# Optimization experiments

Measured on AMD Instinct MI355X. Metric: run time of the kernel, lower is better.

The kernel has to match this reference:

```python
import jax, jax.numpy as jnp
import numpy as np

N = 10000   # nodes
E = 40000   # edges
D = 256     # d_model
H = 32      # num_heads
DK = 16     # d_k == d_v
L = 5       # decoder layers
SQRT_DK = float(np.sqrt(DK))


def layer_norm(x, g, b, eps=1e-5):
    m = x.mean(-1, keepdims=True)
    v = ((x - m) ** 2).mean(-1, keepdims=True)
    return (x - m) / jnp.sqrt(v + eps) * g + b


def mha(x, edge_index, We, Wq, Wk, Wv, Wo, bo):
    # x: [N, D]
    xe = x @ We.T                                   # embed, no bias
    Q = (xe @ Wq.T).reshape(N, H, DK)               # [N, H, dk]
    K = (xe @ Wk.T).reshape(N, H, DK)
    V = (xe @ Wv.T).reshape(N, H, DK)
    src, dst = edge_index[0], edge_index[1]          # message j->i, aggregate at dst
    Qi = Q[dst]                                      # [E, H, dk]
    Kj = K[src]
    Vj = V[src]
    # torch split_heads gives [*, dk, H]; Q_i @ K_j^T contracts over the HEAD axis
    alpha = jnp.einsum('eha,ehb->eab', Qi, Kj) / SQRT_DK   # [E, dk, dk]
    att = jax.nn.softmax(alpha, axis=-1)                    # per-edge softmax over last dk axis
    msg = jnp.einsum('eab,ehb->eah', att, Vj)               # [E, dk, H]
    agg = jax.ops.segment_sum(msg, dst, num_segments=N)     # [N, dk, H] scatter-add
    attn_out = jnp.transpose(agg, (0, 2, 1)).reshape(N, H * DK)  # combine_heads
    # dropout is identity at inference
    return xe + attn_out @ Wo.T + bo


def decoder(edge_index, x, We, Wq, Wk, Wv, Wo, bo, ln_g, ln_b, mlp_W, mlp_b):
    for l in range(L):
        h = mha(x, edge_index, We[l, 0], Wq[l, 0], Wk[l, 0], Wv[l, 0], Wo[l, 0], bo[l, 0])
        x = layer_norm(x + h, ln_g[l, 0], ln_b[l, 0])
        h = mha(x, edge_index, We[l, 1], Wq[l, 1], Wk[l, 1], Wv[l, 1], Wo[l, 1], bo[l, 1])
        x = layer_norm(x + h, ln_g[l, 1], ln_b[l, 1])
        x = layer_norm(x + x @ mlp_W[l].T + mlp_b[l], ln_g[l, 2], ln_b[l, 2])
    return x


def setup_inputs() -> dict:
    key = jax.random.key(0)
    ks = jax.random.split(key, 10)
    s = 0.05
    return {
        'edge_index': jax.random.randint(ks[0], (2, E), 0, N, dtype=jnp.int32),
        'x': jax.random.normal(ks[1], (N, D), dtype=jnp.float32),
        'We': jax.random.normal(ks[2], (L, 2, D, D), dtype=jnp.float32) * s,
        'Wq': jax.random.normal(ks[3], (L, 2, H * DK, D), dtype=jnp.float32) * s,
        'Wk': jax.random.normal(ks[4], (L, 2, H * DK, D), dtype=jnp.float32) * s,
        'Wv': jax.random.normal(ks[5], (L, 2, H * DK, D), dtype=jnp.float32) * s,
        'Wo': jax.random.normal(ks[6], (L, 2, D, H * DK), dtype=jnp.float32) * s,
        'bo': jnp.zeros((L, 2, D), dtype=jnp.float32),
        'ln_g': jnp.ones((L, 3, D), dtype=jnp.float32),
        'ln_b': jnp.zeros((L, 3, D), dtype=jnp.float32),
        'mlp_W': jax.random.normal(ks[7], (L, D, D), dtype=jnp.float32) * s,
        'mlp_b': jnp.zeros((L, D), dtype=jnp.float32),
    }


def reference(edge_index, x, We, Wq, Wk, Wv, Wo, bo, ln_g, ln_b, mlp_W, mlp_b):
    return decoder(edge_index, x, We, Wq, Wk, Wv, Wo, bo, ln_g, ln_b, mlp_W, mlp_b)
```

## Files before the change

### kernel.cpp

```cpp
#include <hip/hip_runtime.h>
#include <hip/hip_bf16.h>

#define N_NODES 10000
#define N_EDGES 40000
#define NLAYERS 5

typedef __bf16 bf16x8 __attribute__((ext_vector_type(8)));
typedef __bf16 bf16x4 __attribute__((ext_vector_type(4)));
typedef float  f32x4  __attribute__((ext_vector_type(4)));

__device__ __forceinline__ bf16x8 cvt8(float4 a, float4 b) {
    bf16x8 r;
    r[0] = (__bf16)a.x; r[1] = (__bf16)a.y; r[2] = (__bf16)a.z; r[3] = (__bf16)a.w;
    r[4] = (__bf16)b.x; r[5] = (__bf16)b.y; r[6] = (__bf16)b.z; r[7] = (__bf16)b.w;
    return r;
}

__device__ __forceinline__ void gload_lds16(const void* g, void* l) {
    __builtin_amdgcn_global_load_lds(
        (const __attribute__((address_space(1))) void*)g,
        (__attribute__((address_space(3))) void*)l, 16, 0, 0);
}

__global__ __launch_bounds__(256) void cvt_chunks(
    const float* __restrict__ s, __bf16* __restrict__ d,
    long chunk, long dstStride, long total8)
{
    for (long i = (long)blockIdx.x * blockDim.x + threadIdx.x; i < total8;
         i += (long)gridDim.x * blockDim.x) {
        long e = i * 8;
        long ch = e / chunk;
        long r  = e - ch * chunk;
        float4 a = *(const float4*)(s + e);
        float4 b = *(const float4*)(s + e + 4);
        *(bf16x8*)(d + ch * dstStride + r) = cvt8(a, b);
    }
}

__global__ __launch_bounds__(256) void cvt_perm_qk(
    const float* __restrict__ S, __bf16* __restrict__ D, long total8)
{
    for (long i = (long)blockIdx.x * blockDim.x + threadIdx.x; i < total8;
         i += (long)gridDim.x * blockDim.x) {
        long e = i * 8;
        int slot = (int)(e >> 17);
        int rem  = (int)(e & 131071);
        int row  = rem >> 8;
        int col  = rem & 255;
        int srow = ((row & 31) << 4) | (row >> 5);
        const float* sp = S + ((long)slot << 17) + ((long)srow << 8) + col;
        float4 a = *(const float4*)sp;
        float4 b = *(const float4*)(sp + 4);
        *(bf16x8*)(D + (long)slot * 393216 + ((long)row << 8) + col) = cvt8(a, b);
    }
}

__global__ __launch_bounds__(256) void transpose_we(
    const float* __restrict__ S, __bf16* __restrict__ D)
{
    __shared__ float tile[64][65];
    const int slot = blockIdx.y;
    const int tx = blockIdx.x & 3, ty = blockIdx.x >> 2;
    const float* sp = S + (size_t)slot * 65536 + (size_t)(ty * 64) * 256 + tx * 64;
    const int t = threadIdx.x;
    #pragma unroll
    for (int j = 0; j < 16; ++j) {
        int idx = t + 256 * j;
        int r = idx >> 6, c = idx & 63;
        tile[r][c] = sp[r * 256 + c];
    }
    __syncthreads();
    __bf16* dp = D + (size_t)slot * 65536 + (size_t)(tx * 64) * 256 + ty * 64;
    #pragma unroll
    for (int j = 0; j < 16; ++j) {
        int idx = t + 256 * j;
        int nl = idx >> 6, kl = idx & 63;
        dp[nl * 256 + kl] = (__bf16)tile[kl][nl];
    }
}

__global__ __launch_bounds__(256) void hist_dst(
    const int* __restrict__ eidx, int* __restrict__ counts)
{
    int e = blockIdx.x * 256 + threadIdx.x;
    if (e < N_EDGES) atomicAdd(&counts[eidx[N_EDGES + e]], 1);
}

__global__ __launch_bounds__(256) void scan_offsets(
    const int* __restrict__ counts, int* __restrict__ offs,
    int* __restrict__ wrk, int n)
{
    const int tid = threadIdx.x;
    const int base = tid * 40;
    int local[40];
    int s = 0;
    #pragma unroll
    for (int j = 0; j < 40; ++j) {
        int i = base + j;
        int v = (i < n) ? counts[i] : 0;
        local[j] = s; s += v;
    }
    __shared__ int sm[256];
    sm[tid] = s;
    __syncthreads();
    for (int off = 1; off < 256; off <<= 1) {
        int t2 = (tid >= off) ? sm[tid - off] : 0;
        __syncthreads();
        sm[tid] += t2;
        __syncthreads();
    }
    int pre = (tid == 0) ? 0 : sm[tid - 1];
    #pragma unroll
    for (int j = 0; j < 40; ++j) {
        int i = base + j;
        if (i < n) { int v = pre + local[j]; offs[i] = v; wrk[i] = v; }
    }
    if (tid == 255) offs[n] = sm[255];
}

__global__ __launch_bounds__(256) void scatter_csr(
    const int* __restrict__ eidx, int* __restrict__ wrk, int* __restrict__ csr_src)
{
    int e = blockIdx.x * 256 + threadIdx.x;
    if (e < N_EDGES) {
        int sn = eidx[e];
        int d  = eidx[N_EDGES + e];
        int pos = atomicAdd(&wrk[d], 1);
        csr_src[pos] = sn;
    }
}

template<int MODE, int BN>
__global__ __launch_bounds__(256) void gemm_lds(
    const __bf16* __restrict__ A, const __bf16* __restrict__ W,
    float* __restrict__ Cf, __bf16* __restrict__ Ch,
    int M, int K, int ldc, long sA, long sW, long sC)
{
    __shared__ __bf16 As[128 * 64];
    __shared__ __bf16 Wsh[BN * 64];
    constexpr int NF = BN / 32;
    A += (long)blockIdx.z * sA;
    W += (long)blockIdx.z * sW;
    if (Ch) Ch += (long)blockIdx.z * sC;
    const int tid = threadIdx.x;
    const int ln  = tid & 63;
    const int wv  = tid >> 6;
    const int wr  = wv >> 1, wc = wv & 1;
    const int brow0 = blockIdx.y * 128;
    const int colb0 = blockIdx.x * BN;

    const int srow = ln >> 3;
    const int scol = ((ln & 7) ^ srow) * 8;
    const int fr = ln & 15;
    const int kq = ln >> 4;
    char* asb = (char*)As;
    char* wsb = (char*)Wsh;

    f32x4 acc[4][NF];
    #pragma unroll
    for (int m = 0; m < 4; ++m)
        #pragma unroll
        for (int n = 0; n < NF; ++n) acc[m][n] = (f32x4){0.f, 0.f, 0.f, 0.f};

    const int nt = K >> 6;
    for (int t = 0; t < nt; ++t) {
        const int kk0 = t << 6;
        if (t) __syncthreads();
        #pragma unroll
        for (int c = 0; c < 4; ++c) {
            int ch = wv * 4 + c;
            int grow = brow0 + ch * 8 + srow;
            if (grow >= M) grow = M - 1;
            gload_lds16(A + (size_t)grow * K + kk0 + scol, asb + ch * 1024);
        }
        #pragma unroll
        for (int c = 0; c < NF; ++c) {
            int ch = wv * NF + c;
            int grow = colb0 + ch * 8 + srow;
            gload_lds16(W + (size_t)grow * K + kk0 + scol, wsb + ch * 1024);
        }
        __syncthreads();
        #pragma unroll
        for (int ks = 0; ks < 2; ++ks) {
            const int kb = ks * 64 + kq * 16;
            const int sw = (fr & 7) << 4;
            bf16x8 af[4], wf[NF];
            #pragma unroll
            for (int m = 0; m < 4; ++m) {
                int row = wr * 64 + m * 16 + fr;
                af[m] = *(const bf16x8*)(asb + row * 128 + (kb ^ sw));
            }
            #pragma unroll
            for (int n = 0; n < NF; ++n) {
                int row = wc * (BN / 2) + n * 16 + fr;
                wf[n] = *(const bf16x8*)(wsb + row * 128 + (kb ^ sw));
            }
            #pragma unroll
            for (int m = 0; m < 4; ++m)
                #pragma unroll
                for (int n = 0; n < NF; ++n)
                    acc[m][n] = __builtin_amdgcn_mfma_f32_16x16x32_bf16(
                        af[m], wf[n], acc[m][n], 0, 0, 0);
        }
    }

    const int rq = (ln >> 4) * 4;
    #pragma unroll
    for (int m = 0; m < 4; ++m) {
        #pragma unroll
        for (int rr = 0; rr < 4; ++rr) {
            int orow = brow0 + wr * 64 + m * 16 + rq + rr;
            if (orow < M) {
                #pragma unroll
                for (int n = 0; n < NF; ++n) {
                    int c = colb0 + wc * (BN / 2) + fr + n * 16;
                    if (MODE == 0)      Cf[(size_t)orow * ldc + c] = acc[m][n][rr];
                    else if (MODE == 1) Ch[(size_t)orow * ldc + c] = (__bf16)acc[m][n][rr];
                    else {
                        if (c < 256) Ch[(size_t)orow * 256 + c] = (__bf16)acc[m][n][rr];
                        else ((__bf16*)Cf)[(size_t)orow * 1536 + (c - 256)] = (__bf16)acc[m][n][rr];
                    }
                }
            }
        }
    }
}

__global__ __launch_bounds__(256) void edge_attn_csr(
    const int* __restrict__ csr_off, const int* __restrict__ csr_src,
    const __bf16* __restrict__ qkv, __bf16* __restrict__ attn_bf)
{
    const int lane = threadIdx.x & 63;
    const int d = blockIdx.x * 4 + (threadIdx.x >> 6);
    const int fr = lane & 15;
    const int G  = lane >> 4;

    const __bf16* qT = qkv + (size_t)d * 1536;
    const bf16x8 qf = *(const bf16x8*)(qT + fr * 32 + G * 8);

    const f32x4 zero = {0.f, 0.f, 0.f, 0.f};
    f32x4 acc0 = zero, acc1 = zero;

    const int i0 = csr_off[d], i1 = csr_off[d + 1];
    for (int i = i0; i < i1; ++i) {
        const int s = csr_src[i];
        const __bf16* kT = qkv + (size_t)s * 1536 + 512;
        const __bf16* vp = qkv + (size_t)s * 1536 + 1024;

        bf16x8 kf = *(const bf16x8*)(kT + fr * 32 + G * 8);
        f32x4 al = __builtin_amdgcn_mfma_f32_16x16x32_bf16(kf, qf, zero, 0, 0, 0);

        float mx = fmaxf(fmaxf(al[0], al[1]), fmaxf(al[2], al[3]));
        mx = fmaxf(mx, __shfl_xor(mx, 16));
        mx = fmaxf(mx, __shfl_xor(mx, 32));
        float p[4];
        #pragma unroll
        for (int r = 0; r < 4; ++r) p[r] = __expf((al[r] - mx) * 0.25f);
        float sum = p[0] + p[1] + p[2] + p[3];
        sum += __shfl_xor(sum, 16);
        sum += __shfl_xor(sum, 32);
        const float inv = 1.f / sum;

        bf16x8 paf;
        #pragma unroll
        for (int j = 0; j < 8; ++j) {
            int srcLane = fr + ((G * 8 + j) >> 2) * 16;
            float v = __shfl(p[j & 3], srcLane);
            paf[j] = (G < 2) ? (__bf16)(v * inv) : (__bf16)0.f;
        }

        bf16x8 vf0 = {0, 0, 0, 0, 0, 0, 0, 0};
        bf16x8 vf1 = {0, 0, 0, 0, 0, 0, 0, 0};
        if (G < 2) {
            vf0 = *(const bf16x8*)(vp + fr * 16 + G * 8);
            vf1 = *(const bf16x8*)(vp + (16 + fr) * 16 + G * 8);
        }
        acc0 = __builtin_amdgcn_mfma_f32_16x16x32_bf16(paf, vf0, acc0, 0, 0, 0);
        acc1 = __builtin_amdgcn_mfma_f32_16x16x32_bf16(paf, vf1, acc1, 0, 0, 0);
    }

    __bf16* ob = attn_bf + (size_t)d * 512;
    bf16x4 o0, o1;
    #pragma unroll
    for (int r = 0; r < 4; ++r) { o0[r] = (__bf16)acc0[r]; o1[r] = (__bf16)acc1[r]; }
    *(bf16x4*)(ob + fr * 16 + G * 4)       = o0;
    *(bf16x4*)(ob + 256 + fr * 16 + G * 4) = o1;
}

template<bool HAS_TB>
__global__ __launch_bounds__(256) void fused_gemm_ln(
    const __bf16* __restrict__ A, const __bf16* __restrict__ W,
    const float* __restrict__ xres, const __bf16* __restrict__ tb,
    const float* __restrict__ bias, const float* __restrict__ g,
    const float* __restrict__ b, float* __restrict__ outf,
    __bf16* __restrict__ outb, int M, int K)
{
    __shared__ __bf16 As[32 * 64];
    __shared__ __bf16 Wsh[256 * 64];
    __shared__ float sm_s[4][32];
    __shared__ float sm_q[4][32];
    const int tid = threadIdx.x;
    const int ln  = tid & 63;
    const int wv  = tid >> 6;
    const int brow0 = blockIdx.x * 32;
    const int srow = ln >> 3;
    const int scol = ((ln & 7) ^ srow) * 8;
    const int fr = ln & 15;
    const int kq = ln >> 4;
    char* asb = (char*)As;
    char* wsb = (char*)Wsh;

    f32x4 acc[2][4];
    #pragma unroll
    for (int m = 0; m < 2; ++m)
        #pragma unroll
        for (int n = 0; n < 4; ++n) acc[m][n] = (f32x4){0.f, 0.f, 0.f, 0.f};

    const int nt = K >> 6;
    for (int t = 0; t < nt; ++t) {
        const int kk0 = t << 6;
        if (t) __syncthreads();
        {
            int grow = brow0 + wv * 8 + srow;
            if (grow >= M) grow = M - 1;
            gload_lds16(A + (size_t)grow * K + kk0 + scol, asb + wv * 1024);
        }
        #pragma unroll
        for (int c = 0; c < 8; ++c) {
            int ch = wv * 8 + c;
            int grow = ch * 8 + srow;
            gload_lds16(W + (size_t)grow * K + kk0 + scol, wsb + ch * 1024);
        }
        __syncthreads();
        #pragma unroll
        for (int ks = 0; ks < 2; ++ks) {
            const int kb = ks * 64 + kq * 16;
            const int sw = (fr & 7) << 4;
            bf16x8 af0 = *(const bf16x8*)(asb + fr * 128 + (kb ^ sw));
            bf16x8 af1 = *(const bf16x8*)(asb + (16 + fr) * 128 + (kb ^ sw));
            #pragma unroll
            for (int n = 0; n < 4; ++n) {
                bf16x8 wf = *(const bf16x8*)(wsb + (wv * 64 + n * 16 + fr) * 128 + (kb ^ sw));
                acc[0][n] = __builtin_amdgcn_mfma_f32_16x16x32_bf16(af0, wf, acc[0][n], 0, 0, 0);
                acc[1][n] = __builtin_amdgcn_mfma_f32_16x16x32_bf16(af1, wf, acc[1][n], 0, 0, 0);
            }
        }
    }

    float s[2][4], q[2][4];
    #pragma unroll
    for (int m = 0; m < 2; ++m)
        #pragma unroll
        for (int rr = 0; rr < 4; ++rr) { s[m][rr] = 0.f; q[m][rr] = 0.f; }
    #pragma unroll
    for (int m = 0; m < 2; ++m)
        #pragma unroll
        for (int n = 0; n < 4; ++n) {
            const int col = wv * 64 + n * 16 + fr;
            const float bi = bias[col];
            #pragma unroll
            for (int rr = 0; rr < 4; ++rr) {
                int gr = brow0 + m * 16 + kq * 4 + rr; if (gr >= M) gr = M - 1;
                float v = acc[m][n][rr] + xres[(size_t)gr * 256 + col] + bi;
                if (HAS_TB) v += (float)tb[(size_t)gr * 256 + col];
                acc[m][n][rr] = v;
                s[m][rr] += v; q[m][rr] += v * v;
            }
        }
    #pragma unroll
    for (int mask = 1; mask < 16; mask <<= 1)
        #pragma unroll
        for (int m = 0; m < 2; ++m)
            #pragma unroll
            for (int rr = 0; rr < 4; ++rr) {
                s[m][rr] += __shfl_xor(s[m][rr], mask);
                q[m][rr] += __shfl_xor(q[m][rr], mask);
            }
    if (fr == 0) {
        #pragma unroll
        for (int m = 0; m < 2; ++m)
            #pragma unroll
            for (int rr = 0; rr < 4; ++rr) {
                sm_s[wv][m * 16 + kq * 4 + rr] = s[m][rr];
                sm_q[wv][m * 16 + kq * 4 + rr] = q[m][rr];
            }
    }
    __syncthreads();
    float mean[2][4], invs[2][4];
    #pragma unroll
    for (int m = 0; m < 2; ++m)
        #pragma unroll
        for (int rr = 0; rr < 4; ++rr) {
            int r = m * 16 + kq * 4 + rr;
            float ts = sm_s[0][r] + sm_s[1][r] + sm_s[2][r] + sm_s[3][r];
            float tq = sm_q[0][r] + sm_q[1][r] + sm_q[2][r] + sm_q[3][r];
            float mn = ts * (1.f / 256.f);
            mean[m][rr] = mn;
            invs[m][rr] = rsqrtf(tq * (1.f / 256.f) - mn * mn + 1e-5f);
        }
    #pragma unroll
    for (int m = 0; m < 2; ++m)
        #pragma unroll
        for (int n = 0; n < 4; ++n) {
            const int col = wv * 64 + n * 16 + fr;
            const float gv = g[col], bv = b[col];
            #pragma unroll
            for (int rr = 0; rr < 4; ++rr) {
                int gr = brow0 + m * 16 + kq * 4 + rr;
                if (gr < M) {
                    float o = (acc[m][n][rr] - mean[m][rr]) * invs[m][rr] * gv + bv;
                    outf[(size_t)gr * 256 + col] = o;
                    outb[(size_t)gr * 256 + col] = (__bf16)o;
                }
            }
        }
}

extern "C" void kernel_launch(void* const* d_in, const int* in_sizes, int n_in,
                              void* d_out, int out_size, void* d_ws, size_t ws_size,
                              hipStream_t stream)
{
    const int*   eidx = (const int*)  d_in[0];
    const float* x_in = (const float*)d_in[1];
    const float* We   = (const float*)d_in[2];
    const float* Wq   = (const float*)d_in[3];
    const float* Wk   = (const float*)d_in[4];
    const float* Wv   = (const float*)d_in[5];
    const float* Wo   = (const float*)d_in[6];
    const float* bo   = (const float*)d_in[7];
    const float* lng  = (const float*)d_in[8];
    const float* lnb  = (const float*)d_in[9];
    const float* mlpW = (const float*)d_in[10];
    const float* mlpb = (const float*)d_in[11];
    float* out = (float*)d_out;

    char* p = (char*)d_ws;
    __bf16* wMerged = (__bf16*)p; p += (size_t)10 * 458752 * 2;
    __bf16* wQKVtmp = (__bf16*)p; p += (size_t)10 * 393216 * 2;
    __bf16* wET     = (__bf16*)p; p += (size_t)10 * 65536  * 2;
    __bf16* wO      = (__bf16*)p; p += (size_t)10 * 131072 * 2;
    __bf16* wM      = (__bf16*)p; p += (size_t)5  * 65536  * 2;
    __bf16* qkv     = (__bf16*)p; p += (size_t)N_NODES * 1536 * 2;
    __bf16* attn_bf = (__bf16*)p; p += (size_t)N_NODES * 512 * 2;
    __bf16* xeb     = (__bf16*)p; p += (size_t)N_NODES * 256 * 2;
    float*  xbf     = (float*) p; p += (size_t)N_NODES * 256 * 4;
    __bf16* xbb     = (__bf16*)p; p += (size_t)N_NODES * 256 * 2;
    int* counts  = (int*)p;    p += (size_t)(N_NODES + 16) * 4;
    int* csr_off = (int*)p;    p += (size_t)(N_NODES + 16) * 4;
    int* csr_wrk = (int*)p;    p += (size_t)(N_NODES + 16) * 4;
    int* csr_src = (int*)p;    p += (size_t)N_EDGES * 4;
    if ((size_t)(p - (char*)d_ws) > ws_size) return;

    dim3 blk(256);
    auto cvtg = [](long total8) { long g = (total8 + 255) / 256; return dim3((unsigned)(g > 2048 ? 2048 : g)); };

    hipMemsetAsync(counts, 0, (size_t)(N_NODES + 16) * 4, stream);
    hist_dst<<<dim3(157), blk, 0, stream>>>(eidx, counts);
    scan_offsets<<<dim3(1), blk, 0, stream>>>(counts, csr_off, csr_wrk, N_NODES);
    scatter_csr<<<dim3(157), blk, 0, stream>>>(eidx, csr_wrk, csr_src);

    cvt_chunks<<<cvtg(81920), blk, 0, stream>>>(We, wMerged, 65536, 458752, 81920);
    cvt_perm_qk<<<cvtg(163840), blk, 0, stream>>>(Wq, wQKVtmp,          163840);
    cvt_perm_qk<<<cvtg(163840), blk, 0, stream>>>(Wk, wQKVtmp + 131072, 163840);
    cvt_chunks<<<cvtg(163840), blk, 0, stream>>>(Wv, wQKVtmp + 262144, 131072, 393216, 163840);
    transpose_we<<<dim3(16, 10), blk, 0, stream>>>(We, wET);
    cvt_chunks<<<cvtg(163840), blk, 0, stream>>>(Wo,  wO, 131072, 131072, 163840);
    cvt_chunks<<<cvtg(40960), blk, 0, stream>>>(mlpW, wM, 65536, 65536, 40960);
    cvt_chunks<<<cvtg(320000), blk, 0, stream>>>(x_in, xbb, 2560000, 2560000, 320000);

    gemm_lds<1, 64><<<dim3(4, 12, 10), blk, 0, stream>>>(
        wQKVtmp, wET, nullptr, wMerged + 65536, 1536, 256, 256,
        393216, 65536, 458752);

    dim3 gMerged(14, 79);

    const float* xcur_f = x_in;
    int step = 0;
    for (int l = 0; l < NLAYERS; ++l) {
        for (int s = 0; s < 2; ++s) {
            size_t ls = (size_t)(l * 2 + s);
            gemm_lds<3, 128><<<gMerged, blk, 0, stream>>>(
                xbb, wMerged + ls * 458752, (float*)qkv, xeb, N_NODES, 256, 0, 0, 0, 0);
            edge_attn_csr<<<dim3(N_NODES / 4), blk, 0, stream>>>(csr_off, csr_src,
                                                                 qkv, attn_bf);
            bool last = (step == 14);
            fused_gemm_ln<true><<<dim3(313), blk, 0, stream>>>(
                attn_bf, wO + ls * 131072, xcur_f, xeb, bo + ls * 256,
                lng + (size_t)(l * 3 + s) * 256, lnb + (size_t)(l * 3 + s) * 256,
                last ? out : xbf, xbb, N_NODES, 512);
            xcur_f = xbf; ++step;
        }
        bool last = (step == 14);
        fused_gemm_ln<false><<<dim3(313), blk, 0, stream>>>(
            xbb, wM + (size_t)l * 65536, xcur_f, nullptr, mlpb + (size_t)l * 256,
            lng + (size_t)(l * 3 + 2) * 256, lnb + (size_t)(l * 3 + 2) * 256,
            last ? out : xbf, xbb, N_NODES, 256);
        xcur_f = xbf; ++step;
    }
}
```

Before: 759.0 us.

## Fuse edge attention into output projection+LayerNorm kernel and merge weight conversions

The per-edge attention kernel is merged into the Wo GEMM + LayerNorm kernel, so each 512-thread block computes attention for 32 destination nodes into LDS and immediately projects and normalizes them. This removes the attn_bf global round trip and one launch per MHA. The MLP GEMM+LN becomes a separate 512-thread kernel that loads A once into LDS and reads W directly from global. The seven weight and input conversion launches are merged into one 2D-grid kernel. In exchange, the fused kernel has only 313 blocks and serializes four nodes' edge loops per wave, which may reduce latency hiding in the gather phase. It also reads W from global without LDS staging.

```diff
diff --git a/kernel.cpp b/kernel.cpp
--- a/kernel.cpp
+++ b/kernel.cpp
@@ -22,36 +22,59 @@
         (__attribute__((address_space(3))) void*)l, 16, 0, 0);
 }
 
-__global__ __launch_bounds__(256) void cvt_chunks(
-    const float* __restrict__ s, __bf16* __restrict__ d,
-    long chunk, long dstStride, long total8)
-{
-    for (long i = (long)blockIdx.x * blockDim.x + threadIdx.x; i < total8;
-         i += (long)gridDim.x * blockDim.x) {
-        long e = i * 8;
-        long ch = e / chunk;
-        long r  = e - ch * chunk;
-        float4 a = *(const float4*)(s + e);
-        float4 b = *(const float4*)(s + e + 4);
-        *(bf16x8*)(d + ch * dstStride + r) = cvt8(a, b);
-    }
-}
-
-__global__ __launch_bounds__(256) void cvt_perm_qk(
-    const float* __restrict__ S, __bf16* __restrict__ D, long total8)
-{
-    for (long i = (long)blockIdx.x * blockDim.x + threadIdx.x; i < total8;
-         i += (long)gridDim.x * blockDim.x) {
-        long e = i * 8;
-        int slot = (int)(e >> 17);
-        int rem  = (int)(e & 131071);
-        int row  = rem >> 8;
-        int col  = rem & 255;
-        int srow = ((row & 31) << 4) | (row >> 5);
-        const float* sp = S + ((long)slot << 17) + ((long)srow << 8) + col;
-        float4 a = *(const float4*)sp;
-        float4 b = *(const float4*)(sp + 4);
-        *(bf16x8*)(D + (long)slot * 393216 + ((long)row << 8) + col) = cvt8(a, b);
+__global__ __launch_bounds__(256) void prep_cvt(
+    const float* __restrict__ We, const float* __restrict__ Wq,
+    const float* __restrict__ Wk, const float* __restrict__ Wv,
+    const float* __restrict__ Wo, const float* __restrict__ mlpW,
+    const float* __restrict__ x_in,
+    __bf16* __restrict__ wMerged, __bf16* __restrict__ wQKVtmp,
+    __bf16* __restrict__ wOd, __bf16* __restrict__ wMd, __bf16* __restrict__ xbb)
+{
+    const int reg = blockIdx.y;
+    long i0 = (long)blockIdx.x * blockDim.x + threadIdx.x;
+    long stride = (long)gridDim.x * blockDim.x;
+    if (reg == 0) {
+        for (long i = i0; i < 81920; i += stride) {
+            long e = i * 8; long ch = e >> 16; long r = e & 65535;
+            *(bf16x8*)(wMerged + ch * 458752 + r) =
+                cvt8(*(const float4*)(We + e), *(const float4*)(We + e + 4));
+        }
+    } else if (reg == 1 || reg == 2) {
+        const float* S = (reg == 1) ? Wq : Wk;
+        __bf16* D = wQKVtmp + ((reg == 2) ? 131072 : 0);
+        for (long i = i0; i < 163840; i += stride) {
+            long e = i * 8;
+            int slot = (int)(e >> 17); int rem = (int)(e & 131071);
+            int row = rem >> 8; int col = rem & 255;
+            int srow = ((row & 31) << 4) | (row >> 5);
+            const float* sp = S + ((long)slot << 17) + ((long)srow << 8) + col;
+            *(bf16x8*)(D + (long)slot * 393216 + ((long)row << 8) + col) =
+                cvt8(*(const float4*)sp, *(const float4*)(sp + 4));
+        }
+    } else if (reg == 3) {
+        for (long i = i0; i < 163840; i += stride) {
+            long e = i * 8; long ch = e >> 17; long r = e & 131071;
+            *(bf16x8*)(wQKVtmp + 262144 + ch * 393216 + r) =
+                cvt8(*(const float4*)(Wv + e), *(const float4*)(Wv + e + 4));
+        }
+    } else if (reg == 4) {
+        for (long i = i0; i < 163840; i += stride) {
+            long e = i * 8;
+            *(bf16x8*)(wOd + e) =
+                cvt8(*(const float4*)(Wo + e), *(const float4*)(Wo + e + 4));
+        }
+    } else if (reg == 5) {
+        for (long i = i0; i < 40960; i += stride) {
+            long e = i * 8;
+            *(bf16x8*)(wMd + e) =
+                cvt8(*(const float4*)(mlpW + e), *(const float4*)(mlpW + e + 4));
+        }
+    } else {
+        for (long i = i0; i < 320000; i += stride) {
+            long e = i * 8;
+            *(bf16x8*)(xbb + e) =
+                cvt8(*(const float4*)(x_in + e), *(const float4*)(x_in + e + 4));
+        }
     }
 }
 
@@ -226,145 +249,123 @@
     }
 }
 
-__global__ __launch_bounds__(256) void edge_attn_csr(
+__global__ __launch_bounds__(512) void mha_tail(
     const int* __restrict__ csr_off, const int* __restrict__ csr_src,
-    const __bf16* __restrict__ qkv, __bf16* __restrict__ attn_bf)
-{
-    const int lane = threadIdx.x & 63;
-    const int d = blockIdx.x * 4 + (threadIdx.x >> 6);
-    const int fr = lane & 15;
-    const int G  = lane >> 4;
-
-    const __bf16* qT = qkv + (size_t)d * 1536;
-    const bf16x8 qf = *(const bf16x8*)(qT + fr * 32 + G * 8);
-
-    const f32x4 zero = {0.f, 0.f, 0.f, 0.f};
-    f32x4 acc0 = zero, acc1 = zero;
-
-    const int i0 = csr_off[d], i1 = csr_off[d + 1];
-    for (int i = i0; i < i1; ++i) {
-        const int s = csr_src[i];
-        const __bf16* kT = qkv + (size_t)s * 1536 + 512;
-        const __bf16* vp = qkv + (size_t)s * 1536 + 1024;
-
-        bf16x8 kf = *(const bf16x8*)(kT + fr * 32 + G * 8);
-        f32x4 al = __builtin_amdgcn_mfma_f32_16x16x32_bf16(kf, qf, zero, 0, 0, 0);
-
-        float mx = fmaxf(fmaxf(al[0], al[1]), fmaxf(al[2], al[3]));
-        mx = fmaxf(mx, __shfl_xor(mx, 16));
-        mx = fmaxf(mx, __shfl_xor(mx, 32));
-        float p[4];
-        #pragma unroll
-        for (int r = 0; r < 4; ++r) p[r] = __expf((al[r] - mx) * 0.25f);
-        float sum = p[0] + p[1] + p[2] + p[3];
-        sum += __shfl_xor(sum, 16);
-        sum += __shfl_xor(sum, 32);
-        const float inv = 1.f / sum;
-
-        bf16x8 paf;
-        #pragma unroll
-        for (int j = 0; j < 8; ++j) {
-            int srcLane = fr + ((G * 8 + j) >> 2) * 16;
-            float v = __shfl(p[j & 3], srcLane);
-            paf[j] = (G < 2) ? (__bf16)(v * inv) : (__bf16)0.f;
-        }
-
-        bf16x8 vf0 = {0, 0, 0, 0, 0, 0, 0, 0};
-        bf16x8 vf1 = {0, 0, 0, 0, 0, 0, 0, 0};
-        if (G < 2) {
-            vf0 = *(const bf16x8*)(vp + fr * 16 + G * 8);
-            vf1 = *(const bf16x8*)(vp + (16 + fr) * 16 + G * 8);
-        }
-        acc0 = __builtin_amdgcn_mfma_f32_16x16x32_bf16(paf, vf0, acc0, 0, 0, 0);
-        acc1 = __builtin_amdgcn_mfma_f32_16x16x32_bf16(paf, vf1, acc1, 0, 0, 0);
-    }
-
-    __bf16* ob = attn_bf + (size_t)d * 512;
-    bf16x4 o0, o1;
-    #pragma unroll
-    for (int r = 0; r < 4; ++r) { o0[r] = (__bf16)acc0[r]; o1[r] = (__bf16)acc1[r]; }
-    *(bf16x4*)(ob + fr * 16 + G * 4)       = o0;
-    *(bf16x4*)(ob + 256 + fr * 16 + G * 4) = o1;
-}
-
-template<bool HAS_TB>
-__global__ __launch_bounds__(256) void fused_gemm_ln(
-    const __bf16* __restrict__ A, const __bf16* __restrict__ W,
+    const __bf16* __restrict__ qkv, const __bf16* __restrict__ W,
     const float* __restrict__ xres, const __bf16* __restrict__ tb,
     const float* __restrict__ bias, const float* __restrict__ g,
     const float* __restrict__ b, float* __restrict__ outf,
-    __bf16* __restrict__ outb, int M, int K)
-{
-    __shared__ __bf16 As[32 * 64];
-    __shared__ __bf16 Wsh[256 * 64];
-    __shared__ float sm_s[4][32];
-    __shared__ float sm_q[4][32];
+    __bf16* __restrict__ outb, int M)
+{
+    __shared__ __bf16 attn_s[32 * 512];
+    __shared__ float sm_s[8][32];
+    __shared__ float sm_q[8][32];
     const int tid = threadIdx.x;
     const int ln  = tid & 63;
     const int wv  = tid >> 6;
+    const int fr  = ln & 15;
+    const int kq  = ln >> 4;
     const int brow0 = blockIdx.x * 32;
-    const int srow = ln >> 3;
-    const int scol = ((ln & 7) ^ srow) * 8;
-    const int fr = ln & 15;
-    const int kq = ln >> 4;
-    char* asb = (char*)As;
-    char* wsb = (char*)Wsh;
-
-    f32x4 acc[2][4];
-    #pragma unroll
-    for (int m = 0; m < 2; ++m)
-        #pragma unroll
-        for (int n = 0; n < 4; ++n) acc[m][n] = (f32x4){0.f, 0.f, 0.f, 0.f};
-
-    const int nt = K >> 6;
-    for (int t = 0; t < nt; ++t) {
-        const int kk0 = t << 6;
-        if (t) __syncthreads();
-        {
-            int grow = brow0 + wv * 8 + srow;
-            if (grow >= M) grow = M - 1;
-            gload_lds16(A + (size_t)grow * K + kk0 + scol, asb + wv * 1024);
-        }
-        #pragma unroll
-        for (int c = 0; c < 8; ++c) {
-            int ch = wv * 8 + c;
-            int grow = ch * 8 + srow;
-            gload_lds16(W + (size_t)grow * K + kk0 + scol, wsb + ch * 1024);
-        }
-        __syncthreads();
+    char* asb = (char*)attn_s;
+    const f32x4 zero = {0.f, 0.f, 0.f, 0.f};
+
+    for (int j = 0; j < 4; ++j) {
+        const int r = wv * 4 + j;
+        const int d = brow0 + r;
+        if (d < M) {
+            const __bf16* qT = qkv + (size_t)d * 1536;
+            const bf16x8 qf = *(const bf16x8*)(qT + fr * 32 + kq * 8);
+            f32x4 acc0 = zero, acc1 = zero;
+            const int i0 = csr_off[d], i1 = csr_off[d + 1];
+            int sN = (i0 < i1) ? csr_src[i0] : 0;
+            bf16x8 kfN = *(const bf16x8*)(qkv + (size_t)sN * 1536 + 512 + fr * 32 + kq * 8);
+            for (int i = i0; i < i1; ++i) {
+                const int s = sN;
+                const bf16x8 kf = kfN;
+                if (i + 1 < i1) {
+                    sN = csr_src[i + 1];
+                    kfN = *(const bf16x8*)(qkv + (size_t)sN * 1536 + 512 + fr * 32 + kq * 8);
+                }
+                const __bf16* vp = qkv + (size_t)s * 1536 + 1024;
+                bf16x8 vf0 = {0, 0, 0, 0, 0, 0, 0, 0};
+                bf16x8 vf1 = {0, 0, 0, 0, 0, 0, 0, 0};
+                if (kq < 2) {
+                    vf0 = *(const bf16x8*)(vp + fr * 16 + kq * 8);
+                    vf1 = *(const bf16x8*)(vp + (16 + fr) * 16 + kq * 8);
+                }
+                f32x4 al = __builtin_amdgcn_mfma_f32_16x16x32_bf16(kf, qf, zero, 0, 0, 0);
+                float mx = fmaxf(fmaxf(al[0], al[1]), fmaxf(al[2], al[3]));
+                mx = fmaxf(mx, __shfl_xor(mx, 16));
+                mx = fmaxf(mx, __shfl_xor(mx, 32));
+                float p[4];
+                #pragma unroll
+                for (int rr = 0; rr < 4; ++rr) p[rr] = __expf((al[rr] - mx) * 0.25f);
+                float sum = p[0] + p[1] + p[2] + p[3];
+                sum += __shfl_xor(sum, 16);
+                sum += __shfl_xor(sum, 32);
+                const float inv = 1.f / sum;
+                bf16x8 paf;
+                #pragma unroll
+                for (int jj = 0; jj < 8; ++jj) {
+                    int srcLane = fr + ((kq * 8 + jj) >> 2) * 16;
+                    float v = __shfl(p[jj & 3], srcLane);
+                    paf[jj] = (kq < 2) ? (__bf16)(v * inv) : (__bf16)0.f;
+                }
+                acc0 = __builtin_amdgcn_mfma_f32_16x16x32_bf16(paf, vf0, acc0, 0, 0, 0);
+                acc1 = __builtin_amdgcn_mfma_f32_16x16x32_bf16(paf, vf1, acc1, 0, 0, 0);
+            }
+            bf16x4 o0, o1;
+            #pragma unroll
+            for (int rr = 0; rr < 4; ++rr) { o0[rr] = (__bf16)acc0[rr]; o1[rr] = (__bf16)acc1[rr]; }
+            const int sw = (r & 7) << 4;
+            *(bf16x4*)(asb + r * 1024 + ((fr * 32 + kq * 8) ^ sw))       = o0;
+            *(bf16x4*)(asb + r * 1024 + ((512 + fr * 32 + kq * 8) ^ sw)) = o1;
+        }
+    }
+    __syncthreads();
+
+    f32x4 acc[2][2];
+    #pragma unroll
+    for (int m = 0; m < 2; ++m)
+        #pragma unroll
+        for (int n = 0; n < 2; ++n) acc[m][n] = zero;
+    const int colw = wv * 32;
+    const int swr = (fr & 7) << 4;
+    #pragma unroll
+    for (int t = 0; t < 8; ++t) {
         #pragma unroll
         for (int ks = 0; ks < 2; ++ks) {
-            const int kb = ks * 64 + kq * 16;
-            const int sw = (fr & 7) << 4;
-            bf16x8 af0 = *(const bf16x8*)(asb + fr * 128 + (kb ^ sw));
-            bf16x8 af1 = *(const bf16x8*)(asb + (16 + fr) * 128 + (kb ^ sw));
-            #pragma unroll
-            for (int n = 0; n < 4; ++n) {
-                bf16x8 wf = *(const bf16x8*)(wsb + (wv * 64 + n * 16 + fr) * 128 + (kb ^ sw));
-                acc[0][n] = __builtin_amdgcn_mfma_f32_16x16x32_bf16(af0, wf, acc[0][n], 0, 0, 0);
-                acc[1][n] = __builtin_amdgcn_mfma_f32_16x16x32_bf16(af1, wf, acc[1][n], 0, 0, 0);
-            }
-        }
-    }
-
-    float s[2][4], q[2][4];
-    #pragma unroll
-    for (int m = 0; m < 2; ++m)
-        #pragma unroll
-        for (int rr = 0; rr < 4; ++rr) { s[m][rr] = 0.f; q[m][rr] = 0.f; }
-    #pragma unroll
-    for (int m = 0; m < 2; ++m)
-        #pragma unroll
-        for (int n = 0; n < 4; ++n) {
-            const int col = wv * 64 + n * 16 + fr;
+            const int kb = t * 128 + ks * 64 + kq * 16;
+            bf16x8 af0 = *(const bf16x8*)(asb + fr * 1024 + (kb ^ swr));
+            bf16x8 af1 = *(const bf16x8*)(asb + (16 + fr) * 1024 + (kb ^ swr));
+            const __bf16* wp = W + (size_t)(colw + fr) * 512 + t * 64 + ks * 32 + kq * 8;
+            bf16x8 wf0 = *(const bf16x8*)wp;
+            bf16x8 wf1 = *(const bf16x8*)(wp + 16 * 512);
+            acc[0][0] = __builtin_amdgcn_mfma_f32_16x16x32_bf16(af0, wf0, acc[0][0], 0, 0, 0);
+            acc[1][0] = __builtin_amdgcn_mfma_f32_16x16x32_bf16(af1, wf0, acc[1][0], 0, 0, 0);
+            acc[0][1] = __builtin_amdgcn_mfma_f32_16x16x32_bf16(af0, wf1, acc[0][1], 0, 0, 0);
+            acc[1][1] = __builtin_amdgcn_mfma_f32_16x16x32_bf16(af1, wf1, acc[1][1], 0, 0, 0);
+        }
+    }
+
+    float s2[2][4], q2[2][4];
+    #pragma unroll
+    for (int m = 0; m < 2; ++m)
+        #pragma unroll
+        for (int rr = 0; rr < 4; ++rr) { s2[m][rr] = 0.f; q2[m][rr] = 0.f; }
+    #pragma unroll
+    for (int m = 0; m < 2; ++m)
+        #pragma unroll
+        for (int n = 0; n < 2; ++n) {
+            const int col = colw + n * 16 + fr;
             const float bi = bias[col];
             #pragma unroll
             for (int rr = 0; rr < 4; ++rr) {
                 int gr = brow0 + m * 16 + kq * 4 + rr; if (gr >= M) gr = M - 1;
-                float v = acc[m][n][rr] + xres[(size_t)gr * 256 + col] + bi;
-                if (HAS_TB) v += (float)tb[(size_t)gr * 256 + col];
+                float v = acc[m][n][rr] + xres[(size_t)gr * 256 + col] + bi
+                          + (float)tb[(size_t)gr * 256 + col];
                 acc[m][n][rr] = v;
-                s[m][rr] += v; q[m][rr] += v * v;
+                s2[m][rr] += v; q2[m][rr] += v * v;
             }
         }
     #pragma unroll
@@ -373,16 +374,16 @@
         for (int m = 0; m < 2; ++m)
             #pragma unroll
             for (int rr = 0; rr < 4; ++rr) {
-                s[m][rr] += __shfl_xor(s[m][rr], mask);
-                q[m][rr] += __shfl_xor(q[m][rr], mask);
+                s2[m][rr] += __shfl_xor(s2[m][rr], mask);
+                q2[m][rr] += __shfl_xor(q2[m][rr], mask);
             }
     if (fr == 0) {
         #pragma unroll
         for (int m = 0; m < 2; ++m)
             #pragma unroll
             for (int rr = 0; rr < 4; ++rr) {
-                sm_s[wv][m * 16 + kq * 4 + rr] = s[m][rr];
-                sm_q[wv][m * 16 + kq * 4 + rr] = q[m][rr];
+                sm_s[wv][m * 16 + kq * 4 + rr] = s2[m][rr];
+                sm_q[wv][m * 16 + kq * 4 + rr] = q2[m][rr];
             }
     }
     __syncthreads();
@@ -391,9 +392,10 @@
     for (int m = 0; m < 2; ++m)
         #pragma unroll
         for (int rr = 0; rr < 4; ++rr) {
-            int r = m * 16 + kq * 4 + rr;
-            float ts = sm_s[0][r] + sm_s[1][r] + sm_s[2][r] + sm_s[3][r];
-            float tq = sm_q[0][r] + sm_q[1][r] + sm_q[2][r] + sm_q[3][r];
+            int rw = m * 16 + kq * 4 + rr;
+            float ts = 0.f, tq = 0.f;
+            #pragma unroll
+            for (int w = 0; w < 8; ++w) { ts += sm_s[w][rw]; tq += sm_q[w][rw]; }
             float mn = ts * (1.f / 256.f);
             mean[m][rr] = mn;
             invs[m][rr] = rsqrtf(tq * (1.f / 256.f) - mn * mn + 1e-5f);
@@ -401,8 +403,131 @@
     #pragma unroll
     for (int m = 0; m < 2; ++m)
         #pragma unroll
-        for (int n = 0; n < 4; ++n) {
-            const int col = wv * 64 + n * 16 + fr;
+        for (int n = 0; n < 2; ++n) {
+            const int col = colw + n * 16 + fr;
+            const float gv = g[col], bv = b[col];
+            #pragma unroll
+            for (int rr = 0; rr < 4; ++rr) {
+                int gr = brow0 + m * 16 + kq * 4 + rr;
+                if (gr < M) {
+                    float o = (acc[m][n][rr] - mean[m][rr]) * invs[m][rr] * gv + bv;
+                    outf[(size_t)gr * 256 + col] = o;
+                    outb[(size_t)gr * 256 + col] = (__bf16)o;
+                }
+            }
+        }
+}
+
+__global__ __launch_bounds__(512) void mlp_fused(
+    const __bf16* __restrict__ A, const __bf16* __restrict__ W,
+    const float* __restrict__ xres, const float* __restrict__ bias,
+    const float* __restrict__ g, const float* __restrict__ b,
+    float* __restrict__ outf, __bf16* __restrict__ outb, int M)
+{
+    __shared__ __bf16 As[32 * 256];
+    __shared__ float sm_s[8][32];
+    __shared__ float sm_q[8][32];
+    const int tid = threadIdx.x;
+    const int ln  = tid & 63;
+    const int wv  = tid >> 6;
+    const int fr  = ln & 15;
+    const int kq  = ln >> 4;
+    const int brow0 = blockIdx.x * 32;
+    char* asb = (char*)As;
+    const f32x4 zero = {0.f, 0.f, 0.f, 0.f};
+
+    const int row2 = ln >> 5;
+    const int bc   = (ln & 31) * 16;
+    #pragma unroll
+    for (int c = 0; c < 2; ++c) {
+        int ch = wv * 2 + c;
+        int r  = ch * 2 + row2;
+        int grow = brow0 + r; if (grow >= M) grow = M - 1;
+        int srcb = bc ^ ((r & 7) << 4);
+        gload_lds16((const char*)A + (size_t)grow * 512 + srcb, asb + ch * 1024);
+    }
+    __syncthreads();
+
+    f32x4 acc[2][2];
+    #pragma unroll
+    for (int m = 0; m < 2; ++m)
+        #pragma unroll
+        for (int n = 0; n < 2; ++n) acc[m][n] = zero;
+    const int colw = wv * 32;
+    const int swr = (fr & 7) << 4;
+    #pragma unroll
+    for (int t = 0; t < 4; ++t) {
+        #pragma unroll
+        for (int ks = 0; ks < 2; ++ks) {
+            const int kb = t * 128 + ks * 64 + kq * 16;
+            bf16x8 af0 = *(const bf16x8*)(asb + fr * 512 + (kb ^ swr));
+            bf16x8 af1 = *(const bf16x8*)(asb + (16 + fr) * 512 + (kb ^ swr));
+            const __bf16* wp = W + (size_t)(colw + fr) * 256 + t * 64 + ks * 32 + kq * 8;
+            bf16x8 wf0 = *(const bf16x8*)wp;
+            bf16x8 wf1 = *(const bf16x8*)(wp + 16 * 256);
+            acc[0][0] = __builtin_amdgcn_mfma_f32_16x16x32_bf16(af0, wf0, acc[0][0], 0, 0, 0);
+            acc[1][0] = __builtin_amdgcn_mfma_f32_16x16x32_bf16(af1, wf0, acc[1][0], 0, 0, 0);
+            acc[0][1] = __builtin_amdgcn_mfma_f32_16x16x32_bf16(af0, wf1, acc[0][1], 0, 0, 0);
+            acc[1][1] = __builtin_amdgcn_mfma_f32_16x16x32_bf16(af1, wf1, acc[1][1], 0, 0, 0);
+        }
+    }
+
+    float s2[2][4], q2[2][4];
+    #pragma unroll
+    for (int m = 0; m < 2; ++m)
+        #pragma unroll
+        for (int rr = 0; rr < 4; ++rr) { s2[m][rr] = 0.f; q2[m][rr] = 0.f; }
+    #pragma unroll
+    for (int m = 0; m < 2; ++m)
+        #pragma unroll
+        for (int n = 0; n < 2; ++n) {
+            const int col = colw + n * 16 + fr;
+            const float bi = bias[col];
+            #pragma unroll
+            for (int rr = 0; rr < 4; ++rr) {
+                int gr = brow0 + m * 16 + kq * 4 + rr; if (gr >= M) gr = M - 1;
+                float v = acc[m][n][rr] + xres[(size_t)gr * 256 + col] + bi;
+                acc[m][n][rr] = v;
+                s2[m][rr] += v; q2[m][rr] += v * v;
+            }
+        }
+    #pragma unroll
+    for (int mask = 1; mask < 16; mask <<= 1)
+        #pragma unroll
+        for (int m = 0; m < 2; ++m)
+            #pragma unroll
+            for (int rr = 0; rr < 4; ++rr) {
+                s2[m][rr] += __shfl_xor(s2[m][rr], mask);
+                q2[m][rr] += __shfl_xor(q2[m][rr], mask);
+            }
+    if (fr == 0) {
+        #pragma unroll
+        for (int m = 0; m < 2; ++m)
+            #pragma unroll
+            for (int rr = 0; rr < 4; ++rr) {
+                sm_s[wv][m * 16 + kq * 4 + rr] = s2[m][rr];
+                sm_q[wv][m * 16 + kq * 4 + rr] = q2[m][rr];
+            }
+    }
+    __syncthreads();
+    float mean[2][4], invs[2][4];
+    #pragma unroll
+    for (int m = 0; m < 2; ++m)
+        #pragma unroll
+        for (int rr = 0; rr < 4; ++rr) {
+            int rw = m * 16 + kq * 4 + rr;
+            float ts = 0.f, tq = 0.f;
+            #pragma unroll
+            for (int w = 0; w < 8; ++w) { ts += sm_s[w][rw]; tq += sm_q[w][rw]; }
+            float mn = ts * (1.f / 256.f);
+            mean[m][rr] = mn;
+            invs[m][rr] = rsqrtf(tq * (1.f / 256.f) - mn * mn + 1e-5f);
+        }
+    #pragma unroll
+    for (int m = 0; m < 2; ++m)
+        #pragma unroll
+        for (int n = 0; n < 2; ++n) {
+            const int col = colw + n * 16 + fr;
             const float gv = g[col], bv = b[col];
             #pragma unroll
             for (int rr = 0; rr < 4; ++rr) {
@@ -441,7 +566,6 @@
     __bf16* wO      = (__bf16*)p; p += (size_t)10 * 131072 * 2;
     __bf16* wM      = (__bf16*)p; p += (size_t)5  * 65536  * 2;
     __bf16* qkv     = (__bf16*)p; p += (size_t)N_NODES * 1536 * 2;
-    __bf16* attn_bf = (__bf16*)p; p += (size_t)N_NODES * 512 * 2;
     __bf16* xeb     = (__bf16*)p; p += (size_t)N_NODES * 256 * 2;
     float*  xbf     = (float*) p; p += (size_t)N_NODES * 256 * 4;
     __bf16* xbb     = (__bf16*)p; p += (size_t)N_NODES * 256 * 2;
@@ -452,21 +576,15 @@
     if ((size_t)(p - (char*)d_ws) > ws_size) return;
 
     dim3 blk(256);
-    auto cvtg = [](long total8) { long g = (total8 + 255) / 256; return dim3((unsigned)(g > 2048 ? 2048 : g)); };
 
     hipMemsetAsync(counts, 0, (size_t)(N_NODES + 16) * 4, stream);
     hist_dst<<<dim3(157), blk, 0, stream>>>(eidx, counts);
     scan_offsets<<<dim3(1), blk, 0, stream>>>(counts, csr_off, csr_wrk, N_NODES);
     scatter_csr<<<dim3(157), blk, 0, stream>>>(eidx, csr_wrk, csr_src);
 
-    cvt_chunks<<<cvtg(81920), blk, 0, stream>>>(We, wMerged, 65536, 458752, 81920);
-    cvt_perm_qk<<<cvtg(163840), blk, 0, stream>>>(Wq, wQKVtmp,          163840);
-    cvt_perm_qk<<<cvtg(163840), blk, 0, stream>>>(Wk, wQKVtmp + 131072, 163840);
-    cvt_chunks<<<cvtg(163840), blk, 0, stream>>>(Wv, wQKVtmp + 262144, 131072, 393216, 163840);
+    prep_cvt<<<dim3(128, 7), blk, 0, stream>>>(We, Wq, Wk, Wv, Wo, mlpW, x_in,
+                                               wMerged, wQKVtmp, wO, wM, xbb);
     transpose_we<<<dim3(16, 10), blk, 0, stream>>>(We, wET);
-    cvt_chunks<<<cvtg(163840), blk, 0, stream>>>(Wo,  wO, 131072, 131072, 163840);
-    cvt_chunks<<<cvtg(40960), blk, 0, stream>>>(mlpW, wM, 65536, 65536, 40960);
-    cvt_chunks<<<cvtg(320000), blk, 0, stream>>>(x_in, xbb, 2560000, 2560000, 320000);
 
     gemm_lds<1, 64><<<dim3(4, 12, 10), blk, 0, stream>>>(
         wQKVtmp, wET, nullptr, wMerged + 65536, 1536, 256, 256,
@@ -481,20 +599,18 @@
             size_t ls = (size_t)(l * 2 + s);
             gemm_lds<3, 128><<<gMerged, blk, 0, stream>>>(
                 xbb, wMerged + ls * 458752, (float*)qkv, xeb, N_NODES, 256, 0, 0, 0, 0);
-            edge_attn_csr<<<dim3(N_NODES / 4), blk, 0, stream>>>(csr_off, csr_src,
-                                                                 qkv, attn_bf);
             bool last = (step == 14);
-            fused_gemm_ln<true><<<dim3(313), blk, 0, stream>>>(
-                attn_bf, wO + ls * 131072, xcur_f, xeb, bo + ls * 256,
+            mha_tail<<<dim3(313), dim3(512), 0, stream>>>(
+                csr_off, csr_src, qkv, wO + ls * 131072, xcur_f, xeb, bo + ls * 256,
                 lng + (size_t)(l * 3 + s) * 256, lnb + (size_t)(l * 3 + s) * 256,
-                last ? out : xbf, xbb, N_NODES, 512);
+                last ? out : xbf, xbb, N_NODES);
             xcur_f = xbf; ++step;
         }
         bool last = (step == 14);
-        fused_gemm_ln<false><<<dim3(313), blk, 0, stream>>>(
-            xbb, wM + (size_t)l * 65536, xcur_f, nullptr, mlpb + (size_t)l * 256,
+        mlp_fused<<<dim3(313), dim3(512), 0, stream>>>(
+            xbb, wM + (size_t)l * 65536, xcur_f, mlpb + (size_t)l * 256,
             lng + (size_t)(l * 3 + 2) * 256, lnb + (size_t)(l * 3 + 2) * 256,
-            last ? out : xbf, xbb, N_NODES, 256);
+            last ? out : xbf, xbb, N_NODES);
         xcur_f = xbf; ++step;
     }
 }
```

Result: slower. 1.069 ms (+40.9%).
